# Kernel optimization log

Hardware: AMD Instinct MI355X
Metric: run time of the kernel (lower is better)

The kernel has to match this reference:

```python
import jax, jax.numpy as jnp
import numpy as np

D_MODEL = 2048
NUM_Q_HEADS = 32
NUM_KV_HEADS = 8
HEAD_SIZE = 64
GROUP_SIZE = NUM_Q_HEADS // NUM_KV_HEADS
B, T = 2, 2048


def setup_inputs() -> dict:
    key = jax.random.key(0)
    k0, k1, k2, k3 = jax.random.split(key, 4)
    std = 1.0 / np.sqrt(D_MODEL)
    x = jax.random.normal(k0, (B, T, D_MODEL), dtype=jnp.float32)
    Wq = jax.random.normal(k1, (D_MODEL, NUM_Q_HEADS * HEAD_SIZE), dtype=jnp.float32) * std
    Wk = jax.random.normal(k2, (D_MODEL, NUM_KV_HEADS * HEAD_SIZE), dtype=jnp.float32) * std
    Wv = jax.random.normal(k3, (D_MODEL, NUM_KV_HEADS * HEAD_SIZE), dtype=jnp.float32) * std
    return {"x": x, "Wq": Wq, "Wk": Wk, "Wv": Wv}


def reference(x, Wq, Wk, Wv):
    Bs, Ts, _ = x.shape
    scale = jnp.sqrt(jnp.asarray(HEAD_SIZE, dtype=x.dtype))
    # projections -> [B, H, T, D]
    q = (x @ Wq).reshape(Bs, Ts, NUM_Q_HEADS, HEAD_SIZE).transpose(0, 2, 1, 3)
    k = (x @ Wk).reshape(Bs, Ts, NUM_KV_HEADS, HEAD_SIZE).transpose(0, 2, 1, 3)
    v = (x @ Wv).reshape(Bs, Ts, NUM_KV_HEADS, HEAD_SIZE).transpose(0, 2, 1, 3)
    # repeat kv heads to match q heads (GQA)
    k = jnp.repeat(k, GROUP_SIZE, axis=1)  # [B, Hq, T, D]
    v = jnp.repeat(v, GROUP_SIZE, axis=1)
    scores = jnp.einsum('bhqd,bhkd->bhqk', q, k) / scale  # [B, Hq, T, T]
    causal = jnp.tril(jnp.ones((Ts, Ts), dtype=bool))
    scores = jnp.where(causal, scores, -jnp.inf)
    attn = jax.nn.softmax(scores, axis=-1)
    out = jnp.einsum('bhqk,bhkd->bhqd', attn, v)  # [B, Hq, T, D]
    return out.transpose(0, 2, 1, 3).reshape(Bs, Ts, NUM_Q_HEADS * HEAD_SIZE)
```

## Files before the change

kernel.cpp:

```cpp
#include <hip/hip_runtime.h>

typedef float floatx4 __attribute__((ext_vector_type(4)));
typedef short shortx8 __attribute__((ext_vector_type(8)));

#define T_SEQ 2048
#define NQH   32
#define NKVH  8
#define HD    64
#define DM    2048
#define NTOT  3072

#if __has_builtin(__builtin_amdgcn_exp2f)
#define EXP2F(x) __builtin_amdgcn_exp2f(x)
#else
#define EXP2F(x) exp2f(x)
#endif

__device__ __forceinline__ unsigned short f2bf(float f) {
    unsigned int u = __builtin_bit_cast(unsigned int, f);
    u += 0x7FFFu + ((u >> 16) & 1u);
    return (unsigned short)(u >> 16);
}
__device__ __forceinline__ unsigned int pk2bf(float a, float b) {
    return (unsigned int)f2bf(a) | ((unsigned int)f2bf(b) << 16);
}

__device__ __forceinline__ void dma16(const unsigned short* g, unsigned short* l) {
    __builtin_amdgcn_global_load_lds(
        (const __attribute__((address_space(1))) unsigned int*)g,
        (__attribute__((address_space(3))) unsigned int*)l,
        16, 0, 0);
}

__global__ __launch_bounds__(256) void cvt_fused(
    const float* __restrict__ x, const float* __restrict__ Wq,
    const float* __restrict__ Wk, const float* __restrict__ Wv,
    unsigned short* __restrict__ xb, unsigned short* __restrict__ wt)
{
    __shared__ __align__(16) unsigned short Ts[64][72];
    const int id = blockIdx.x;
    const int t = threadIdx.x;
    if (id < 4096) {
        size_t i = ((size_t)id * 256 + t) * 8;
        float4 a = *(const float4*)(x + i);
        float4 b = *(const float4*)(x + i + 4);
        uint4 o;
        o.x = pk2bf(a.x, a.y); o.y = pk2bf(a.z, a.w);
        o.z = pk2bf(b.x, b.y); o.w = pk2bf(b.z, b.w);
        *(uint4*)(xb + i) = o;
        return;
    }
    const int id2 = id - 4096;
    const int k0 = (id2 & 31) * 64, n0g = (id2 >> 5) * 64;
    const float* W; int ldW, col0;
    if (n0g < 2048)      { W = Wq; ldW = 2048; col0 = n0g; }
    else if (n0g < 2560) { W = Wk; ldW = 512;  col0 = n0g - 2048; }
    else                 { W = Wv; ldW = 512;  col0 = n0g - 2560; }
    {
        int r = t >> 2, c = (t & 3) * 16;
        const float* src = W + (size_t)(k0 + r) * ldW + col0 + c;
        float4 v0 = *(const float4*)(src);
        float4 v1 = *(const float4*)(src + 4);
        float4 v2 = *(const float4*)(src + 8);
        float4 v3 = *(const float4*)(src + 12);
        uint4 o0 = {pk2bf(v0.x, v0.y), pk2bf(v0.z, v0.w), pk2bf(v1.x, v1.y), pk2bf(v1.z, v1.w)};
        uint4 o1 = {pk2bf(v2.x, v2.y), pk2bf(v2.z, v2.w), pk2bf(v3.x, v3.y), pk2bf(v3.z, v3.w)};
        *(uint4*)&Ts[r][c]     = o0;
        *(uint4*)&Ts[r][c + 8] = o1;
    }
    __syncthreads();
    {
        int n = t >> 2, kc = (t & 3) * 16;
        unsigned int dw[8];
        #pragma unroll
        for (int i = 0; i < 8; i++)
            dw[i] = (unsigned int)Ts[kc + 2 * i][n] | ((unsigned int)Ts[kc + 2 * i + 1][n] << 16);
        uint4 o0 = {dw[0], dw[1], dw[2], dw[3]}, o1 = {dw[4], dw[5], dw[6], dw[7]};
        unsigned short* d = wt + (size_t)(n0g + n) * DM + k0 + kc;
        *(uint4*)d = o0; *(uint4*)(d + 8) = o1;
    }
}

__global__ __launch_bounds__(256, 4) void qkv_gemm(
    const unsigned short* __restrict__ xb,
    const unsigned short* __restrict__ wt,
    unsigned short* __restrict__ Qws, unsigned short* __restrict__ Kws,
    unsigned short* __restrict__ Vws)
{
    __shared__ __align__(16) unsigned short At[128 * 64];
    __shared__ __align__(16) unsigned short Bt[128 * 64];

    const int tid = threadIdx.x;
    const int wave = tid >> 6, lane = tid & 63;
    const int l16 = lane & 15, qd = lane >> 4;

    const int id  = blockIdx.y * 24 + blockIdx.x;
    const int xcd = id & 7, j = id >> 3;
    const int m0 = (xcd * 4 + (j & 3)) * 128;
    const int n0 = (j >> 2) * 128;

    const int mh = (wave >> 1) * 64, nh = (wave & 1) * 64;

    const int lrow = lane >> 3;
    const int cgw  = (lane & 7) ^ lrow;
    const int cg0  = (qd ^ (l16 & 7)) * 8;
    const int cg1  = ((4 | qd) ^ (l16 & 7)) * 8;

    floatx4 acc[4][4];
    #pragma unroll
    for (int mi = 0; mi < 4; mi++)
        #pragma unroll
        for (int ni = 0; ni < 4; ni++)
            acc[mi][ni] = (floatx4){0.f, 0.f, 0.f, 0.f};

    size_t gA[4], gB[4];
    int lofs[4];
    #pragma unroll
    for (int jj = 0; jj < 4; jj++) {
        const int rb = wave * 32 + jj * 8;
        gA[jj] = (size_t)(m0 + rb + lrow) * DM + cgw * 8;
        gB[jj] = (size_t)(n0 + rb + lrow) * DM + cgw * 8;
        lofs[jj] = rb * 64;
    }

    #pragma unroll
    for (int jj = 0; jj < 4; jj++) {
        dma16(xb + gA[jj], &At[lofs[jj]]);
        dma16(wt + gB[jj], &Bt[lofs[jj]]);
    }

    for (int k0 = 0; k0 < DM; k0 += 64) {
        __syncthreads();
        #pragma unroll
        for (int ks = 0; ks < 2; ks++) {
            const int cg = ks ? cg1 : cg0;
            shortx8 af[4], bfr[4];
            #pragma unroll
            for (int i = 0; i < 4; i++) {
                af[i]  = *(const shortx8*)&At[(mh + i * 16 + l16) * 64 + cg];
                bfr[i] = *(const shortx8*)&Bt[(nh + i * 16 + l16) * 64 + cg];
            }
            #pragma unroll
            for (int mi = 0; mi < 4; mi++)
                #pragma unroll
                for (int ni = 0; ni < 4; ni++)
                    acc[mi][ni] = __builtin_amdgcn_mfma_f32_16x16x32_bf16(
                        af[mi], bfr[ni], acc[mi][ni], 0, 0, 0);
        }
        __syncthreads();
        if (k0 + 64 < DM) {
            #pragma unroll
            for (int jj = 0; jj < 4; jj++) {
                dma16(xb + gA[jj] + k0 + 64, &At[lofs[jj]]);
                dma16(wt + gB[jj] + k0 + 64, &Bt[lofs[jj]]);
            }
        }
    }

    int ncol, H; unsigned short* dst; float sc; bool vtrans;
    if (n0 < 2048)      { ncol = n0;        dst = Qws; H = NQH;  sc = 0.125f * 1.44269504f; vtrans = false; }
    else if (n0 < 2560) { ncol = n0 - 2048; dst = Kws; H = NKVH; sc = 1.0f; vtrans = false; }
    else                { ncol = n0 - 2560; dst = Vws; H = NKVH; sc = 1.0f; vtrans = true;  }

    #pragma unroll
    for (int mi = 0; mi < 4; mi++)
        #pragma unroll
        for (int ni = 0; ni < 4; ni++)
            #pragma unroll
            for (int r = 0; r < 4; r++) {
                int m  = m0 + mh + mi * 16 + qd * 4 + r;
                int nc = ncol + nh + ni * 16 + l16;
                int b  = m >> 11, t = m & (T_SEQ - 1);
                int hh = nc >> 6, d = nc & 63;
                float v = acc[mi][ni][r] * sc;
                size_t idx = vtrans
                    ? ((((size_t)b * H + hh) * HD + d) << 11) + t
                    : ((((size_t)b * H + hh) * T_SEQ + t) << 6) + d;
                dst[idx] = f2bf(v);
            }
}

__global__ __launch_bounds__(256, 2) void attn_fwd(
    const unsigned short* __restrict__ Qws,
    const unsigned short* __restrict__ Kws,
    const unsigned short* __restrict__ Vtws,
    float* __restrict__ out)
{
    __shared__ __align__(16) unsigned short Ks[2][64 * 64];
    __shared__ __align__(16) unsigned short Vt[2][64 * 64];
    __shared__ __align__(16) unsigned short Ps[4][64][40];

    const int tid = threadIdx.x;
    const int wave = tid >> 6, lane = tid & 63;
    const int l16 = lane & 15, qd = lane >> 4;
    const int b = blockIdx.z;
    const int qt = b ? blockIdx.x : (31 - blockIdx.x);
    const int kh = blockIdx.y;
    const int h = kh * 4 + wave;
    const int q0 = qt * 64;

    const size_t qbase  = (((size_t)b * NQH + h) * T_SEQ + q0) * HD;
    const size_t kbase  = ((size_t)b * NKVH + kh) * (size_t)T_SEQ * HD;
    const size_t vtbase = ((size_t)b * NKVH + kh) * (size_t)HD * T_SEQ;

    shortx8 qfr[4][2];
    #pragma unroll
    for (int mqt = 0; mqt < 4; mqt++)
        #pragma unroll
        for (int ks = 0; ks < 2; ks++)
            qfr[mqt][ks] = *(const shortx8*)(Qws + qbase +
                (size_t)(mqt * 16 + l16) * HD + ks * 32 + qd * 8);

    floatx4 oaccT[4][4];
    #pragma unroll
    for (int mqt = 0; mqt < 4; mqt++)
        #pragma unroll
        for (int dt = 0; dt < 4; dt++)
            oaccT[mqt][dt] = (floatx4){0.f, 0.f, 0.f, 0.f};
    float lsum[4] = {0.f, 0.f, 0.f, 0.f};

    const int lrow = lane >> 3;
    const int cgw  = (lane & 7) ^ lrow;
    const int xr   = l16 & 7;

    #pragma unroll
    for (int j2 = 0; j2 < 2; j2++) {
        const int rb = wave * 16 + j2 * 8;
        dma16(Kws  + kbase  + (size_t)(rb + lrow) * HD + cgw * 8, &Ks[0][rb * 64]);
        dma16(Vtws + vtbase + (size_t)(rb + lrow) * T_SEQ + cgw * 8, &Vt[0][rb * 64]);
    }

    for (int c = 0; c <= qt; c++) {
        const int cur = c & 1;
        const int j0 = c * 64;
        __syncthreads();
        if (c < qt) {
            const int j0n = j0 + 64;
            #pragma unroll
            for (int j2 = 0; j2 < 2; j2++) {
                const int rb = wave * 16 + j2 * 8;
                dma16(Kws  + kbase  + (size_t)(j0n + rb + lrow) * HD + cgw * 8,
                      &Ks[cur ^ 1][rb * 64]);
                dma16(Vtws + vtbase + (size_t)(rb + lrow) * T_SEQ + j0n + cgw * 8,
                      &Vt[cur ^ 1][rb * 64]);
            }
        }

        const bool diag = (c == qt);

        #pragma unroll
        for (int kp = 0; kp < 2; kp++) {
            shortx8 kf[2][2];
            #pragma unroll
            for (int ktl = 0; ktl < 2; ktl++) {
                const int krow = ((kp * 2 + ktl) * 16 + l16) * 64;
                kf[ktl][0] = *(const shortx8*)&Ks[cur][krow + ((qd ^ xr) * 8)];
                kf[ktl][1] = *(const shortx8*)&Ks[cur][krow + (((4 | qd) ^ xr) * 8)];
            }

            #pragma unroll
            for (int ktl = 0; ktl < 2; ktl++) {
                #pragma unroll
                for (int mqt = 0; mqt < 4; mqt++) {
                    floatx4 s = (floatx4){0.f, 0.f, 0.f, 0.f};
                    s = __builtin_amdgcn_mfma_f32_16x16x32_bf16(kf[ktl][0], qfr[mqt][0], s, 0, 0, 0);
                    s = __builtin_amdgcn_mfma_f32_16x16x32_bf16(kf[ktl][1], qfr[mqt][1], s, 0, 0, 0);
                    unsigned int pu[4];
                    if (diag) {
                        const int qrel = mqt * 16 + l16;
                        const int jbase = kp * 32 + ktl * 16 + qd * 4;
                        #pragma unroll
                        for (int r = 0; r < 4; r++) {
                            float pe = EXP2F(s[r]);
                            unsigned int u = __builtin_bit_cast(unsigned int, pe) & 0xFFFF0000u;
                            if (jbase + r > qrel) u = 0u;
                            pu[r] = u;
                            lsum[mqt] += __builtin_bit_cast(float, u);
                        }
                    } else {
                        #pragma unroll
                        for (int r = 0; r < 4; r++) {
                            float pe = EXP2F(s[r]);
                            unsigned int u = __builtin_bit_cast(unsigned int, pe) & 0xFFFF0000u;
                            pu[r] = u;
                            lsum[mqt] += __builtin_bit_cast(float, u);
                        }
                    }
                    uint2 dw;
                    dw.x = (pu[0] >> 16) | (pu[1] & 0xFFFF0000u);
                    dw.y = (pu[2] >> 16) | (pu[3] & 0xFFFF0000u);
                    *(uint2*)&Ps[wave][mqt * 16 + l16][ktl * 16 + qd * 4] = dw;
                }
            }

            shortx8 pfr[4];
            #pragma unroll
            for (int mqt = 0; mqt < 4; mqt++)
                pfr[mqt] = *(const shortx8*)&Ps[wave][mqt * 16 + l16][qd * 8];

            #pragma unroll
            for (int dt = 0; dt < 4; dt++) {
                const shortx8 vf = *(const shortx8*)
                    &Vt[cur][(dt * 16 + l16) * 64 + (((kp * 4 + qd) ^ xr) * 8)];
                #pragma unroll
                for (int mqt = 0; mqt < 4; mqt++)
                    oaccT[mqt][dt] = __builtin_amdgcn_mfma_f32_16x16x32_bf16(
                        vf, pfr[mqt], oaccT[mqt][dt], 0, 0, 0);
            }
        }
    }

    float inv[4];
    #pragma unroll
    for (int mqt = 0; mqt < 4; mqt++) {
        float s = lsum[mqt];
        s += __shfl_xor(s, 16, 64);
        s += __shfl_xor(s, 32, 64);
        inv[mqt] = 1.f / s;
    }

    #pragma unroll
    for (int mqt = 0; mqt < 4; mqt++) {
        const int t = q0 + mqt * 16 + l16;
        float* orow = out + ((size_t)b * T_SEQ + t) * (NQH * HD) + h * HD + qd * 4;
        #pragma unroll
        for (int dt = 0; dt < 4; dt++) {
            float4 o;
            o.x = oaccT[mqt][dt][0] * inv[mqt];
            o.y = oaccT[mqt][dt][1] * inv[mqt];
            o.z = oaccT[mqt][dt][2] * inv[mqt];
            o.w = oaccT[mqt][dt][3] * inv[mqt];
            *(float4*)(orow + dt * 16) = o;
        }
    }
}

extern "C" void kernel_launch(void* const* d_in, const int* in_sizes, int n_in,
                              void* d_out, int out_size, void* d_ws, size_t ws_size,
                              hipStream_t stream) {
    const float* x  = (const float*)d_in[0];
    const float* Wq = (const float*)d_in[1];
    const float* Wk = (const float*)d_in[2];
    const float* Wv = (const float*)d_in[3];
    float* out = (float*)d_out;

    unsigned short* xb  = (unsigned short*)d_out;
    unsigned short* wt  = (unsigned short*)d_ws;
    unsigned short* Qws = wt  + (size_t)NTOT * DM;
    unsigned short* Kws = Qws + (size_t)2 * NQH * T_SEQ * HD;
    unsigned short* Vws = Kws + (size_t)2 * NKVH * T_SEQ * HD;

    cvt_fused<<<4096 + 1536, 256, 0, stream>>>(x, Wq, Wk, Wv, xb, wt);
    qkv_gemm <<<dim3(24, 32), 256, 0, stream>>>(xb, wt, Qws, Kws, Vws);
    attn_fwd <<<dim3(32, NKVH, 2), 256, 0, stream>>>(Qws, Kws, Vws, out);
}
```

Baseline: 227.1 us.

## Split attention query rows across 8 waves and compute row sums via MFMA

Attention blocks grow from 256 to 512 threads, and each wave now handles 32 query rows instead of 64 for one head. This halves per-wave accumulator registers and doubles the waves per block. Row sums of P move from scalar adds to an MFMA against a ones vector. P is converted with the hardware packed bf16 convert, so it is rounded rather than truncated. Masked-out diagonal subtiles are skipped, and MFMA priority is raised around the PV multiply. Each K/V tile is now loaded by 8 waves, but there are fewer blocks per CU by register budget, and the extra MFMA adds some work.

```diff
diff --git a/kernel.cpp b/kernel.cpp
--- a/kernel.cpp
+++ b/kernel.cpp
@@ -23,6 +23,12 @@
 }
 __device__ __forceinline__ unsigned int pk2bf(float a, float b) {
     return (unsigned int)f2bf(a) | ((unsigned int)f2bf(b) << 16);
+}
+
+__device__ __forceinline__ unsigned int cvtpk_bf16(float lo, float hi) {
+    unsigned int r;
+    asm("v_cvt_pk_bf16_f32 %0, %1, %2" : "=v"(r) : "v"(lo), "v"(hi));
+    return r;
 }
 
 __device__ __forceinline__ void dma16(const unsigned short* g, unsigned short* l) {
@@ -180,7 +186,7 @@
             }
 }
 
-__global__ __launch_bounds__(256, 2) void attn_fwd(
+__global__ __launch_bounds__(512, 4) void attn_fwd(
     const unsigned short* __restrict__ Qws,
     const unsigned short* __restrict__ Kws,
     const unsigned short* __restrict__ Vtws,
@@ -188,140 +194,134 @@
 {
     __shared__ __align__(16) unsigned short Ks[2][64 * 64];
     __shared__ __align__(16) unsigned short Vt[2][64 * 64];
-    __shared__ __align__(16) unsigned short Ps[4][64][40];
+    __shared__ __align__(16) unsigned short Ps[8][32][40];
 
     const int tid = threadIdx.x;
     const int wave = tid >> 6, lane = tid & 63;
+    const int whead = wave & 3, wrow = wave >> 2;
     const int l16 = lane & 15, qd = lane >> 4;
     const int b = blockIdx.z;
     const int qt = b ? blockIdx.x : (31 - blockIdx.x);
     const int kh = blockIdx.y;
-    const int h = kh * 4 + wave;
+    const int h = kh * 4 + whead;
     const int q0 = qt * 64;
+    const int mh = wrow * 32;
 
     const size_t qbase  = (((size_t)b * NQH + h) * T_SEQ + q0) * HD;
     const size_t kbase  = ((size_t)b * NKVH + kh) * (size_t)T_SEQ * HD;
     const size_t vtbase = ((size_t)b * NKVH + kh) * (size_t)HD * T_SEQ;
 
-    shortx8 qfr[4][2];
-    #pragma unroll
-    for (int mqt = 0; mqt < 4; mqt++)
+    shortx8 qfr[2][2];
+    #pragma unroll
+    for (int mqt = 0; mqt < 2; mqt++)
         #pragma unroll
         for (int ks = 0; ks < 2; ks++)
             qfr[mqt][ks] = *(const shortx8*)(Qws + qbase +
-                (size_t)(mqt * 16 + l16) * HD + ks * 32 + qd * 8);
-
-    floatx4 oaccT[4][4];
-    #pragma unroll
-    for (int mqt = 0; mqt < 4; mqt++)
+                (size_t)(mh + mqt * 16 + l16) * HD + ks * 32 + qd * 8);
+
+    const shortx8 ones = {0x3F80, 0x3F80, 0x3F80, 0x3F80,
+                          0x3F80, 0x3F80, 0x3F80, 0x3F80};
+
+    floatx4 oaccT[2][4];
+    #pragma unroll
+    for (int mqt = 0; mqt < 2; mqt++)
         #pragma unroll
         for (int dt = 0; dt < 4; dt++)
             oaccT[mqt][dt] = (floatx4){0.f, 0.f, 0.f, 0.f};
-    float lsum[4] = {0.f, 0.f, 0.f, 0.f};
+    floatx4 psum[2];
+    psum[0] = (floatx4){0.f, 0.f, 0.f, 0.f};
+    psum[1] = (floatx4){0.f, 0.f, 0.f, 0.f};
 
     const int lrow = lane >> 3;
     const int cgw  = (lane & 7) ^ lrow;
     const int xr   = l16 & 7;
-
-    #pragma unroll
-    for (int j2 = 0; j2 < 2; j2++) {
-        const int rb = wave * 16 + j2 * 8;
-        dma16(Kws  + kbase  + (size_t)(rb + lrow) * HD + cgw * 8, &Ks[0][rb * 64]);
-        dma16(Vtws + vtbase + (size_t)(rb + lrow) * T_SEQ + cgw * 8, &Vt[0][rb * 64]);
-    }
+    const int rb   = wave * 8;
+
+    dma16(Kws  + kbase  + (size_t)(rb + lrow) * HD + cgw * 8, &Ks[0][rb * 64]);
+    dma16(Vtws + vtbase + (size_t)(rb + lrow) * T_SEQ + cgw * 8, &Vt[0][rb * 64]);
 
     for (int c = 0; c <= qt; c++) {
         const int cur = c & 1;
-        const int j0 = c * 64;
         __syncthreads();
         if (c < qt) {
-            const int j0n = j0 + 64;
-            #pragma unroll
-            for (int j2 = 0; j2 < 2; j2++) {
-                const int rb = wave * 16 + j2 * 8;
-                dma16(Kws  + kbase  + (size_t)(j0n + rb + lrow) * HD + cgw * 8,
-                      &Ks[cur ^ 1][rb * 64]);
-                dma16(Vtws + vtbase + (size_t)(rb + lrow) * T_SEQ + j0n + cgw * 8,
-                      &Vt[cur ^ 1][rb * 64]);
+            const int j0n = (c + 1) * 64;
+            dma16(Kws  + kbase  + (size_t)(j0n + rb + lrow) * HD + cgw * 8,
+                  &Ks[cur ^ 1][rb * 64]);
+            dma16(Vtws + vtbase + (size_t)(rb + lrow) * T_SEQ + j0n + cgw * 8,
+                  &Vt[cur ^ 1][rb * 64]);
+        }
+
+        const bool diag = (c == qt);
+
+        #pragma unroll
+        for (int kp = 0; kp < 2; kp++) {
+            if (!(diag && wrow == 0 && kp == 1)) {
+                shortx8 kf[2][2];
+                #pragma unroll
+                for (int ktl = 0; ktl < 2; ktl++) {
+                    const int krow = ((kp * 2 + ktl) * 16 + l16) * 64;
+                    kf[ktl][0] = *(const shortx8*)&Ks[cur][krow + ((qd ^ xr) * 8)];
+                    kf[ktl][1] = *(const shortx8*)&Ks[cur][krow + (((4 | qd) ^ xr) * 8)];
+                }
+
+                const bool msk = diag && (wrow == kp);
+
+                #pragma unroll
+                for (int ktl = 0; ktl < 2; ktl++) {
+                    #pragma unroll
+                    for (int mqt = 0; mqt < 2; mqt++) {
+                        floatx4 s = (floatx4){0.f, 0.f, 0.f, 0.f};
+                        s = __builtin_amdgcn_mfma_f32_16x16x32_bf16(kf[ktl][0], qfr[mqt][0], s, 0, 0, 0);
+                        s = __builtin_amdgcn_mfma_f32_16x16x32_bf16(kf[ktl][1], qfr[mqt][1], s, 0, 0, 0);
+                        float pe[4];
+                        #pragma unroll
+                        for (int r = 0; r < 4; r++) pe[r] = EXP2F(s[r]);
+                        if (msk) {
+                            const int qrel  = mh + mqt * 16 + l16;
+                            const int jbase = kp * 32 + ktl * 16 + qd * 4;
+                            #pragma unroll
+                            for (int r = 0; r < 4; r++)
+                                if (jbase + r > qrel) pe[r] = 0.f;
+                        }
+                        uint2 dw;
+                        dw.x = cvtpk_bf16(pe[0], pe[1]);
+                        dw.y = cvtpk_bf16(pe[2], pe[3]);
+                        *(uint2*)&Ps[wave][mqt * 16 + l16][ktl * 16 + qd * 4] = dw;
+                    }
+                }
+
+                shortx8 pfr[2];
+                #pragma unroll
+                for (int mqt = 0; mqt < 2; mqt++)
+                    pfr[mqt] = *(const shortx8*)&Ps[wave][mqt * 16 + l16][qd * 8];
+
+                #pragma unroll
+                for (int mqt = 0; mqt < 2; mqt++)
+                    psum[mqt] = __builtin_amdgcn_mfma_f32_16x16x32_bf16(
+                        ones, pfr[mqt], psum[mqt], 0, 0, 0);
+
+                __builtin_amdgcn_s_setprio(1);
+                #pragma unroll
+                for (int dt = 0; dt < 4; dt++) {
+                    const shortx8 vf = *(const shortx8*)
+                        &Vt[cur][(dt * 16 + l16) * 64 + (((kp * 4 + qd) ^ xr) * 8)];
+                    #pragma unroll
+                    for (int mqt = 0; mqt < 2; mqt++)
+                        oaccT[mqt][dt] = __builtin_amdgcn_mfma_f32_16x16x32_bf16(
+                            vf, pfr[mqt], oaccT[mqt][dt], 0, 0, 0);
+                }
+                __builtin_amdgcn_s_setprio(0);
             }
         }
-
-        const bool diag = (c == qt);
-
-        #pragma unroll
-        for (int kp = 0; kp < 2; kp++) {
-            shortx8 kf[2][2];
-            #pragma unroll
-            for (int ktl = 0; ktl < 2; ktl++) {
-                const int krow = ((kp * 2 + ktl) * 16 + l16) * 64;
-                kf[ktl][0] = *(const shortx8*)&Ks[cur][krow + ((qd ^ xr) * 8)];
-                kf[ktl][1] = *(const shortx8*)&Ks[cur][krow + (((4 | qd) ^ xr) * 8)];
-            }
-
-            #pragma unroll
-            for (int ktl = 0; ktl < 2; ktl++) {
-                #pragma unroll
-                for (int mqt = 0; mqt < 4; mqt++) {
-                    floatx4 s = (floatx4){0.f, 0.f, 0.f, 0.f};
-                    s = __builtin_amdgcn_mfma_f32_16x16x32_bf16(kf[ktl][0], qfr[mqt][0], s, 0, 0, 0);
-                    s = __builtin_amdgcn_mfma_f32_16x16x32_bf16(kf[ktl][1], qfr[mqt][1], s, 0, 0, 0);
-                    unsigned int pu[4];
-                    if (diag) {
-                        const int qrel = mqt * 16 + l16;
-                        const int jbase = kp * 32 + ktl * 16 + qd * 4;
-                        #pragma unroll
-                        for (int r = 0; r < 4; r++) {
-                            float pe = EXP2F(s[r]);
-                            unsigned int u = __builtin_bit_cast(unsigned int, pe) & 0xFFFF0000u;
-                            if (jbase + r > qrel) u = 0u;
-                            pu[r] = u;
-                            lsum[mqt] += __builtin_bit_cast(float, u);
-                        }
-                    } else {
-                        #pragma unroll
-                        for (int r = 0; r < 4; r++) {
-                            float pe = EXP2F(s[r]);
-                            unsigned int u = __builtin_bit_cast(unsigned int, pe) & 0xFFFF0000u;
-                            pu[r] = u;
-                            lsum[mqt] += __builtin_bit_cast(float, u);
-                        }
-                    }
-                    uint2 dw;
-                    dw.x = (pu[0] >> 16) | (pu[1] & 0xFFFF0000u);
-                    dw.y = (pu[2] >> 16) | (pu[3] & 0xFFFF0000u);
-                    *(uint2*)&Ps[wave][mqt * 16 + l16][ktl * 16 + qd * 4] = dw;
-                }
-            }
-
-            shortx8 pfr[4];
-            #pragma unroll
-            for (int mqt = 0; mqt < 4; mqt++)
-                pfr[mqt] = *(const shortx8*)&Ps[wave][mqt * 16 + l16][qd * 8];
-
-            #pragma unroll
-            for (int dt = 0; dt < 4; dt++) {
-                const shortx8 vf = *(const shortx8*)
-                    &Vt[cur][(dt * 16 + l16) * 64 + (((kp * 4 + qd) ^ xr) * 8)];
-                #pragma unroll
-                for (int mqt = 0; mqt < 4; mqt++)
-                    oaccT[mqt][dt] = __builtin_amdgcn_mfma_f32_16x16x32_bf16(
-                        vf, pfr[mqt], oaccT[mqt][dt], 0, 0, 0);
-            }
-        }
-    }
-
-    float inv[4];
-    #pragma unroll
-    for (int mqt = 0; mqt < 4; mqt++) {
-        float s = lsum[mqt];
-        s += __shfl_xor(s, 16, 64);
-        s += __shfl_xor(s, 32, 64);
-        inv[mqt] = 1.f / s;
-    }
-
-    #pragma unroll
-    for (int mqt = 0; mqt < 4; mqt++) {
-        const int t = q0 + mqt * 16 + l16;
+    }
+
+    float inv[2];
+    inv[0] = 1.f / psum[0][0];
+    inv[1] = 1.f / psum[1][0];
+
+    #pragma unroll
+    for (int mqt = 0; mqt < 2; mqt++) {
+        const int t = q0 + mh + mqt * 16 + l16;
         float* orow = out + ((size_t)b * T_SEQ + t) * (NQH * HD) + h * HD + qd * 4;
         #pragma unroll
         for (int dt = 0; dt < 4; dt++) {
@@ -352,5 +352,5 @@
 
     cvt_fused<<<4096 + 1536, 256, 0, stream>>>(x, Wq, Wk, Wv, xb, wt);
     qkv_gemm <<<dim3(24, 32), 256, 0, stream>>>(xb, wt, Qws, Kws, Vws);
-    attn_fwd <<<dim3(32, NKVH, 2), 256, 0, stream>>>(Qws, Kws, Vws, out);
-}
+    attn_fwd <<<dim3(32, NKVH, 2), 512, 0, stream>>>(Qws, Kws, Vws, out);
+}
```

Result: faster. 213.4 us (-6.0%).
